# Optimization experiments

Hardware: AMD Instinct MI355X
Metric: run time of the kernel (lower is better)

The kernel has to match this reference:

```python
import jax, jax.numpy as jnp
import numpy as np

ITERATION = 10

def setup_inputs() -> dict:
    key = jax.random.key(0)
    k1, k2, k3 = jax.random.split(key, 3)
    a_inter = jax.random.normal(k1, (8, 64, 64, 32, 32), dtype=jnp.float32)
    logits = jax.random.normal(k2, (8, 64), dtype=jnp.float32)
    W = jax.random.normal(k3, (1, 64, 64), dtype=jnp.float32)
    return {"a_inter": a_inter, "logits": logits, "W": W}


def reference(a_inter, logits, W):
    N = W.shape[1]  # num_nodes
    B = a_inter.shape[0]
    # feats: [B, N, C*H*W]
    feats = a_inter[:, :, :N, :, :].reshape(B, N, -1)
    # expand logits [B, N] -> [B, N, N] (unsqueeze(1).expand in torch)
    logits0 = jnp.broadcast_to(logits[:, None, :], (B, N, N))

    feats_norm = jnp.linalg.norm(feats, ord=2, axis=2, keepdims=True)  # [B, N, 1]
    pairwise_norm = feats_norm @ jnp.swapaxes(feats_norm, 1, 2)        # [B, N, N]
    pairwise_dot = feats @ jnp.swapaxes(feats, 1, 2)                   # [B, N, N]
    pairwise_sim = pairwise_dot / (pairwise_norm + 1e-6)
    W_sym = (W + jnp.swapaxes(W, 1, 2)) / 2.0
    pairwise_potential = pairwise_sim * W_sym                          # [B, N, N]

    unary_potential = logits0

    def body(i, l):
        probs = jnp.swapaxes(jax.nn.sigmoid(l), 1, 2)  # [B, N, N]
        # probs*pp - (1-probs)*pp == (2*probs - 1)*pp
        pp_E = jnp.sum((2.0 * probs - 1.0) * pairwise_potential, axis=2, keepdims=True)
        return unary_potential + pp_E

    logits_out = jax.lax.fori_loop(0, ITERATION, body, logits0)
    return logits_out.mean(axis=1)  # [B, N]
```

## Files before the change

kernel.cpp:

```cpp
#include <hip/hip_runtime.h>
#include <math.h>

#define BATCH 8
#define NN 64
#define DD 65536
#define BPB 64
#define NBLK (BATCH * BPB)
#define KC (DD / BPB)
#define KW (KC / 4)
#define KSTEPS (KW / 32)
#define NTRI 10
#define PSZ (NTRI * 256)

typedef float  floatx4 __attribute__((ext_vector_type(4)));
typedef __bf16 bf16x8  __attribute__((ext_vector_type(8)));

static __device__ __forceinline__ bf16x8 cvt8(float4 lo, float4 hi) {
    const unsigned sel = 0x07060302u;
    union { unsigned u[4]; bf16x8 v; } r;
    r.u[0] = __builtin_amdgcn_perm(__float_as_uint(lo.y), __float_as_uint(lo.x), sel);
    r.u[1] = __builtin_amdgcn_perm(__float_as_uint(lo.w), __float_as_uint(lo.z), sel);
    r.u[2] = __builtin_amdgcn_perm(__float_as_uint(hi.y), __float_as_uint(hi.x), sel);
    r.u[3] = __builtin_amdgcn_perm(__float_as_uint(hi.w), __float_as_uint(hi.z), sel);
    return r.v;
}

__global__ __launch_bounds__(256, 3) void gram_partial_kernel(const float* __restrict__ a,
                                                              float* __restrict__ part) {
    __shared__ __align__(16) float red[3][NTRI][64][4];

    const int bid = blockIdx.x;
    const int b = bid >> 6;
    const int c = bid & (BPB - 1);

    const int tid  = threadIdx.x;
    const int w    = tid >> 6;
    const int lane = tid & 63;
    const int m    = lane & 15;
    const int q    = lane >> 4;

    const float* base = a + (size_t)b * NN * DD + (size_t)c * KC + (size_t)w * KW
                          + (size_t)m * DD + q * 8;
    const float* p0 = base;
    const float* p1 = base + (size_t)16 * DD;
    const float* p2 = base + (size_t)32 * DD;
    const float* p3 = base + (size_t)48 * DD;

    floatx4 acc[NTRI];
    #pragma unroll
    for (int i = 0; i < NTRI; ++i) acc[i] = (floatx4)0.0f;

    float4 A0, A1, A2, A3, A4, A5, A6, A7;
    float4 B0, B1, B2, B3, B4, B5, B6, B7;

#define LOADSET(R0,R1,R2,R3,R4,R5,R6,R7, o)                                \
    R0 = *(const float4*)(p0 + (o));  R1 = *(const float4*)(p0 + (o) + 4); \
    R2 = *(const float4*)(p1 + (o));  R3 = *(const float4*)(p1 + (o) + 4); \
    R4 = *(const float4*)(p2 + (o));  R5 = *(const float4*)(p2 + (o) + 4); \
    R6 = *(const float4*)(p3 + (o));  R7 = *(const float4*)(p3 + (o) + 4);

#define MFMASET(R0,R1,R2,R3,R4,R5,R6,R7)                                   \
    {                                                                      \
        bf16x8 f0 = cvt8(R0, R1);                                          \
        bf16x8 f1 = cvt8(R2, R3);                                          \
        bf16x8 f2 = cvt8(R4, R5);                                          \
        bf16x8 f3 = cvt8(R6, R7);                                          \
        acc[0] = __builtin_amdgcn_mfma_f32_16x16x32_bf16(f0, f0, acc[0], 0, 0, 0); \
        acc[1] = __builtin_amdgcn_mfma_f32_16x16x32_bf16(f0, f1, acc[1], 0, 0, 0); \
        acc[2] = __builtin_amdgcn_mfma_f32_16x16x32_bf16(f0, f2, acc[2], 0, 0, 0); \
        acc[3] = __builtin_amdgcn_mfma_f32_16x16x32_bf16(f0, f3, acc[3], 0, 0, 0); \
        acc[4] = __builtin_amdgcn_mfma_f32_16x16x32_bf16(f1, f1, acc[4], 0, 0, 0); \
        acc[5] = __builtin_amdgcn_mfma_f32_16x16x32_bf16(f1, f2, acc[5], 0, 0, 0); \
        acc[6] = __builtin_amdgcn_mfma_f32_16x16x32_bf16(f1, f3, acc[6], 0, 0, 0); \
        acc[7] = __builtin_amdgcn_mfma_f32_16x16x32_bf16(f2, f2, acc[7], 0, 0, 0); \
        acc[8] = __builtin_amdgcn_mfma_f32_16x16x32_bf16(f2, f3, acc[8], 0, 0, 0); \
        acc[9] = __builtin_amdgcn_mfma_f32_16x16x32_bf16(f3, f3, acc[9], 0, 0, 0); \
    }

    LOADSET(A0,A1,A2,A3,A4,A5,A6,A7, 0)
    #pragma unroll
    for (int s = 0; s < KSTEPS; s += 2) {
        LOADSET(B0,B1,B2,B3,B4,B5,B6,B7, (s + 1) * 32)
        MFMASET(A0,A1,A2,A3,A4,A5,A6,A7)
        if (s + 2 < KSTEPS) { LOADSET(A0,A1,A2,A3,A4,A5,A6,A7, (s + 2) * 32) }
        MFMASET(B0,B1,B2,B3,B4,B5,B6,B7)
    }
#undef LOADSET
#undef MFMASET

    if (w > 0) {
        #pragma unroll
        for (int t = 0; t < NTRI; ++t)
            *(floatx4*)&red[w - 1][t][lane][0] = acc[t];
    }
    __syncthreads();
    if (w == 0) {
        #pragma unroll
        for (int t = 0; t < NTRI; ++t) {
            floatx4 r0 = *(const floatx4*)&red[0][t][lane][0];
            floatx4 r1 = *(const floatx4*)&red[1][t][lane][0];
            floatx4 r2 = *(const floatx4*)&red[2][t][lane][0];
            acc[t] += (r0 + r1) + r2;
        }
        float* pg = part + (size_t)bid * PSZ;
        #pragma unroll
        for (int t = 0; t < NTRI; ++t) {
            float* tp = pg + t * 256 + m;
            #pragma unroll
            for (int r = 0; r < 4; ++r)
                tp[(q * 4 + r) * 16] = acc[t][r];
        }
    }
}

__global__ __launch_bounds__(128) void gram_reduce_kernel(const float* __restrict__ part,
                                                          float* __restrict__ gram) {
    const int gid = blockIdx.x * 128 + threadIdx.x;
    const int b   = gid >> 12;
    const int idx = gid & 4095;
    const int i   = idx >> 6;
    const int j   = idx & 63;
    const int ti  = i >> 4, tj = j >> 4;
    const int ib  = ti <= tj ? ti : tj;
    const int jb  = ti <= tj ? tj : ti;
    const int slot = ib * 4 - (ib * (ib - 1)) / 2 + (jb - ib);
    const int rr  = (ti <= tj) ? (i & 15) : (j & 15);
    const int cc  = (ti <= tj) ? (j & 15) : (i & 15);
    const int off = slot * 256 + rr * 16 + cc;
    const float* p = part + (size_t)b * BPB * PSZ + off;

    float s0 = 0.f, s1 = 0.f, s2 = 0.f, s3 = 0.f;
    #pragma unroll 4
    for (int c = 0; c < BPB; c += 4) {
        s0 += p[(size_t)(c + 0) * PSZ];
        s1 += p[(size_t)(c + 1) * PSZ];
        s2 += p[(size_t)(c + 2) * PSZ];
        s3 += p[(size_t)(c + 3) * PSZ];
    }
    gram[gid] = (s0 + s1) + (s2 + s3);
}

__global__ __launch_bounds__(256) void crf_kernel(const float* __restrict__ gram,
                                                  const float* __restrict__ logits,
                                                  const float* __restrict__ Wm,
                                                  float* __restrict__ out) {
    __shared__ float pp[NN][NN + 1];
    __shared__ float E[NN];
    __shared__ float nrm[NN];
    __shared__ float part[4 * NN];

    const int b  = blockIdx.x;
    const int tid = threadIdx.x;
    const int i  = tid & 63;
    const int jq = tid >> 6;
    const float* g = gram + b * NN * NN;

    if (jq == 0) nrm[i] = sqrtf(g[i * NN + i]);
    E[i] = 0.0f;
    __syncthreads();

    const float ni = nrm[i];
    for (int jj = 0; jj < 16; ++jj) {
        int j = jq * 16 + jj;
        float wsym = 0.5f * (Wm[i * NN + j] + Wm[j * NN + i]);
        pp[i][j] = g[i * NN + j] / (ni * nrm[j] + 1e-6f) * wsym;
    }
    const float li = logits[b * NN + i];
    __syncthreads();

    for (int it = 0; it < 10; ++it) {
        float acc = 0.0f;
        for (int jj = 0; jj < 16; ++jj) {
            int j = jq * 16 + jj;
            float t = li + E[j];
            float s = 1.0f / (1.0f + expf(-t));
            acc = fmaf(2.0f * s - 1.0f, pp[i][j], acc);
        }
        part[jq * NN + i] = acc;
        __syncthreads();
        if (jq == 0)
            E[i] = part[i] + part[NN + i] + part[2 * NN + i] + part[3 * NN + i];
        __syncthreads();
    }

    if (tid < 64) {
        float s = E[tid];
        for (int off = 32; off > 0; off >>= 1) s += __shfl_down(s, off);
        float meanE = __shfl(s, 0) * (1.0f / 64.0f);
        out[b * NN + tid] = logits[b * NN + tid] + meanE;
    }
}

extern "C" void kernel_launch(void* const* d_in, const int* in_sizes, int n_in,
                              void* d_out, int out_size, void* d_ws, size_t ws_size,
                              hipStream_t stream) {
    const float* a      = (const float*)d_in[0];
    const float* logits = (const float*)d_in[1];
    const float* Wm     = (const float*)d_in[2];
    float* out  = (float*)d_out;

    float* part = (float*)d_ws;
    float* gram = part + (size_t)NBLK * PSZ;

    gram_partial_kernel<<<NBLK, 256, 0, stream>>>(a, part);
    gram_reduce_kernel<<<(BATCH * NN * NN) / 128, 128, 0, stream>>>(part, gram);
    crf_kernel<<<BATCH, 256, 0, stream>>>(gram, logits, Wm, out);
}
```

Measured before the change: 217.7 us.

## Fuse gram reduction and CRF into partial kernel via atomics and last-block

Replaces the separate partial-store, reduce and CRF kernels with one fused kernel. Each block atomically adds its partial Gram tile into a per-batch accumulator, and the last block for each batch, found through an atomic counter, runs the CRF iterations. A small init kernel zeroes the accumulator and counters. This removes two launches and the partial-buffer round trip, at the cost of float atomics (non-deterministic summation order) and a serial CRF tail on a single block per batch.

After: 235.6 us. 1.08x slower.

```diff
diff --git a/kernel.cpp b/kernel.cpp
--- a/kernel.cpp
+++ b/kernel.cpp
@@ -11,6 +11,8 @@
 #define KSTEPS (KW / 32)
 #define NTRI 10
 #define PSZ (NTRI * 256)
+#define GRAM_FLOATS (BATCH * PSZ)
+#define INIT_N (GRAM_FLOATS + BATCH)
 
 typedef float  floatx4 __attribute__((ext_vector_type(4)));
 typedef __bf16 bf16x8  __attribute__((ext_vector_type(8)));
@@ -25,9 +27,26 @@
     return r.v;
 }
 
-__global__ __launch_bounds__(256, 3) void gram_partial_kernel(const float* __restrict__ a,
-                                                              float* __restrict__ part) {
-    __shared__ __align__(16) float red[3][NTRI][64][4];
+__global__ __launch_bounds__(256) void init_kernel(float* __restrict__ g) {
+    int i = blockIdx.x * 256 + threadIdx.x;
+    if (i < INIT_N) g[i] = 0.0f;
+}
+
+__global__ __launch_bounds__(256, 3) void fused_kernel(const float* __restrict__ a,
+                                                       const float* __restrict__ logits,
+                                                       const float* __restrict__ Wm,
+                                                       float* __restrict__ gram,
+                                                       float* __restrict__ out) {
+    __shared__ __align__(16) union {
+        float red[3][NTRI][64][4];
+        struct {
+            float G[NN][NN + 1];
+            float E[NN];
+            float nrm[NN];
+            float part[4 * NN];
+        } crf;
+    } sh;
+    __shared__ int lastFlag;
 
     const int bid = blockIdx.x;
     const int b = bid >> 6;
@@ -91,100 +110,86 @@
     if (w > 0) {
         #pragma unroll
         for (int t = 0; t < NTRI; ++t)
-            *(floatx4*)&red[w - 1][t][lane][0] = acc[t];
+            *(floatx4*)&sh.red[w - 1][t][lane][0] = acc[t];
     }
     __syncthreads();
     if (w == 0) {
         #pragma unroll
         for (int t = 0; t < NTRI; ++t) {
-            floatx4 r0 = *(const floatx4*)&red[0][t][lane][0];
-            floatx4 r1 = *(const floatx4*)&red[1][t][lane][0];
-            floatx4 r2 = *(const floatx4*)&red[2][t][lane][0];
+            floatx4 r0 = *(const floatx4*)&sh.red[0][t][lane][0];
+            floatx4 r1 = *(const floatx4*)&sh.red[1][t][lane][0];
+            floatx4 r2 = *(const floatx4*)&sh.red[2][t][lane][0];
             acc[t] += (r0 + r1) + r2;
         }
-        float* pg = part + (size_t)bid * PSZ;
+        float* pg = gram + (size_t)b * PSZ;
         #pragma unroll
         for (int t = 0; t < NTRI; ++t) {
             float* tp = pg + t * 256 + m;
             #pragma unroll
             for (int r = 0; r < 4; ++r)
-                tp[(q * 4 + r) * 16] = acc[t][r];
+                atomicAdd(&tp[(q * 4 + r) * 16], acc[t][r]);
         }
-    }
-}
-
-__global__ __launch_bounds__(128) void gram_reduce_kernel(const float* __restrict__ part,
-                                                          float* __restrict__ gram) {
-    const int gid = blockIdx.x * 128 + threadIdx.x;
-    const int b   = gid >> 12;
-    const int idx = gid & 4095;
-    const int i   = idx >> 6;
-    const int j   = idx & 63;
-    const int ti  = i >> 4, tj = j >> 4;
-    const int ib  = ti <= tj ? ti : tj;
-    const int jb  = ti <= tj ? tj : ti;
-    const int slot = ib * 4 - (ib * (ib - 1)) / 2 + (jb - ib);
-    const int rr  = (ti <= tj) ? (i & 15) : (j & 15);
-    const int cc  = (ti <= tj) ? (j & 15) : (i & 15);
-    const int off = slot * 256 + rr * 16 + cc;
-    const float* p = part + (size_t)b * BPB * PSZ + off;
-
-    float s0 = 0.f, s1 = 0.f, s2 = 0.f, s3 = 0.f;
-    #pragma unroll 4
-    for (int c = 0; c < BPB; c += 4) {
-        s0 += p[(size_t)(c + 0) * PSZ];
-        s1 += p[(size_t)(c + 1) * PSZ];
-        s2 += p[(size_t)(c + 2) * PSZ];
-        s3 += p[(size_t)(c + 3) * PSZ];
-    }
-    gram[gid] = (s0 + s1) + (s2 + s3);
-}
-
-__global__ __launch_bounds__(256) void crf_kernel(const float* __restrict__ gram,
-                                                  const float* __restrict__ logits,
-                                                  const float* __restrict__ Wm,
-                                                  float* __restrict__ out) {
-    __shared__ float pp[NN][NN + 1];
-    __shared__ float E[NN];
-    __shared__ float nrm[NN];
-    __shared__ float part[4 * NN];
-
-    const int b  = blockIdx.x;
-    const int tid = threadIdx.x;
-    const int i  = tid & 63;
+        __threadfence();
+    }
+    if (tid == 0) {
+        unsigned* cnt = (unsigned*)(gram + GRAM_FLOATS);
+        unsigned old = atomicAdd(cnt + b, 1u);
+        lastFlag = (old == BPB - 1) ? 1 : 0;
+    }
+    __syncthreads();
+    if (!lastFlag) return;
+
+    const float* gb = gram + (size_t)b * PSZ;
+    for (int idx = tid; idx < NN * NN; idx += 256) {
+        int i  = idx >> 6, j = idx & 63;
+        int ti = i >> 4, tj = j >> 4;
+        int ib = ti <= tj ? ti : tj;
+        int jb = ti <= tj ? tj : ti;
+        int slot = ib * 4 - (ib * (ib - 1)) / 2 + (jb - ib);
+        int rr = (ti <= tj) ? (i & 15) : (j & 15);
+        int cc = (ti <= tj) ? (j & 15) : (i & 15);
+        float v = __hip_atomic_load(gb + slot * 256 + rr * 16 + cc,
+                                    __ATOMIC_RELAXED, __HIP_MEMORY_SCOPE_AGENT);
+        sh.crf.G[i][j] = v;
+    }
+    __syncthreads();
+
+    const int ci = tid & 63;
     const int jq = tid >> 6;
-    const float* g = gram + b * NN * NN;
-
-    if (jq == 0) nrm[i] = sqrtf(g[i * NN + i]);
-    E[i] = 0.0f;
-    __syncthreads();
-
-    const float ni = nrm[i];
+
+    if (jq == 0) sh.crf.nrm[ci] = sqrtf(sh.crf.G[ci][ci]);
+    sh.crf.E[ci] = 0.0f;
+    __syncthreads();
+
+    const float ni = sh.crf.nrm[ci];
+    #pragma unroll
     for (int jj = 0; jj < 16; ++jj) {
         int j = jq * 16 + jj;
-        float wsym = 0.5f * (Wm[i * NN + j] + Wm[j * NN + i]);
-        pp[i][j] = g[i * NN + j] / (ni * nrm[j] + 1e-6f) * wsym;
-    }
-    const float li = logits[b * NN + i];
+        float wsym = 0.5f * (Wm[ci * NN + j] + Wm[j * NN + ci]);
+        sh.crf.G[ci][j] = sh.crf.G[ci][j] / (ni * sh.crf.nrm[j] + 1e-6f) * wsym;
+    }
+    const float li = logits[b * NN + ci];
     __syncthreads();
 
     for (int it = 0; it < 10; ++it) {
-        float acc = 0.0f;
+        float acc2 = 0.0f;
+        #pragma unroll
         for (int jj = 0; jj < 16; ++jj) {
             int j = jq * 16 + jj;
-            float t = li + E[j];
+            float t = li + sh.crf.E[j];
             float s = 1.0f / (1.0f + expf(-t));
-            acc = fmaf(2.0f * s - 1.0f, pp[i][j], acc);
+            acc2 = fmaf(2.0f * s - 1.0f, sh.crf.G[ci][j], acc2);
         }
-        part[jq * NN + i] = acc;
+        sh.crf.part[jq * NN + ci] = acc2;
         __syncthreads();
         if (jq == 0)
-            E[i] = part[i] + part[NN + i] + part[2 * NN + i] + part[3 * NN + i];
+            sh.crf.E[ci] = sh.crf.part[ci] + sh.crf.part[NN + ci]
+                         + sh.crf.part[2 * NN + ci] + sh.crf.part[3 * NN + ci];
         __syncthreads();
     }
 
     if (tid < 64) {
-        float s = E[tid];
+        float s = sh.crf.E[tid];
         for (int off = 32; off > 0; off >>= 1) s += __shfl_down(s, off);
         float meanE = __shfl(s, 0) * (1.0f / 64.0f);
         out[b * NN + tid] = logits[b * NN + tid] + meanE;
@@ -199,10 +204,8 @@
     const float* Wm     = (const float*)d_in[2];
     float* out  = (float*)d_out;
 
-    float* part = (float*)d_ws;
-    float* gram = part + (size_t)NBLK * PSZ;
-
-    gram_partial_kernel<<<NBLK, 256, 0, stream>>>(a, part);
-    gram_reduce_kernel<<<(BATCH * NN * NN) / 128, 128, 0, stream>>>(part, gram);
-    crf_kernel<<<BATCH, 256, 0, stream>>>(gram, logits, Wm, out);
-}
+    float* gram = (float*)d_ws;
+
+    init_kernel<<<(INIT_N + 255) / 256, 256, 0, stream>>>(gram);
+    fused_kernel<<<NBLK, 256, 0, stream>>>(a, logits, Wm, gram, out);
+}
```

## Split Gram partials per wave and drop the in-block LDS reduction

Applied to the files above, without the earlier changes.

The Gram partial kernel now launches 2048 blocks of 128 threads instead of 512 blocks of 256. Each wave covers a 128-element K slice and writes its own partial tile straight to global memory, so the shared-memory reduction and its barrier are gone. The reduce kernel now sums 512 partials per batch instead of 64, using eight accumulators. The aim is more waves in flight to hide load latency, but the partial buffer grows eightfold, adding a lot of global write and read traffic plus a longer strided reduction.

New measurement: 261.1 us. 19.9% more time.

```diff
diff --git a/kernel.cpp b/kernel.cpp
--- a/kernel.cpp
+++ b/kernel.cpp
@@ -4,11 +4,11 @@
 #define BATCH 8
 #define NN 64
 #define DD 65536
-#define BPB 64
-#define NBLK (BATCH * BPB)
-#define KC (DD / BPB)
-#define KW (KC / 4)
-#define KSTEPS (KW / 32)
+#define NBLK 2048
+#define WPB 512
+#define NWAVE (BATCH * WPB)
+#define KWV 128
+#define KSTEPS (KWV / 32)
 #define NTRI 10
 #define PSZ (NTRI * 256)
 
@@ -25,21 +25,18 @@
     return r.v;
 }
 
-__global__ __launch_bounds__(256, 3) void gram_partial_kernel(const float* __restrict__ a,
+__global__ __launch_bounds__(128, 4) void gram_partial_kernel(const float* __restrict__ a,
                                                               float* __restrict__ part) {
-    __shared__ __align__(16) float red[3][NTRI][64][4];
-
-    const int bid = blockIdx.x;
-    const int b = bid >> 6;
-    const int c = bid & (BPB - 1);
-
+    const int bid  = blockIdx.x;
+    const int b    = bid >> 8;
     const int tid  = threadIdx.x;
     const int w    = tid >> 6;
     const int lane = tid & 63;
     const int m    = lane & 15;
     const int q    = lane >> 4;
+    const int c    = ((bid & 255) << 1) | w;
 
-    const float* base = a + (size_t)b * NN * DD + (size_t)c * KC + (size_t)w * KW
+    const float* base = a + (size_t)b * NN * DD + (size_t)c * KWV
                           + (size_t)m * DD + q * 8;
     const float* p0 = base;
     const float* p1 = base + (size_t)16 * DD;
@@ -88,28 +85,13 @@
 #undef LOADSET
 #undef MFMASET
 
-    if (w > 0) {
+    float* pg = part + ((size_t)b * WPB + c) * PSZ;
+    #pragma unroll
+    for (int t = 0; t < NTRI; ++t) {
+        float* tp = pg + t * 256 + m;
         #pragma unroll
-        for (int t = 0; t < NTRI; ++t)
-            *(floatx4*)&red[w - 1][t][lane][0] = acc[t];
-    }
-    __syncthreads();
-    if (w == 0) {
-        #pragma unroll
-        for (int t = 0; t < NTRI; ++t) {
-            floatx4 r0 = *(const floatx4*)&red[0][t][lane][0];
-            floatx4 r1 = *(const floatx4*)&red[1][t][lane][0];
-            floatx4 r2 = *(const floatx4*)&red[2][t][lane][0];
-            acc[t] += (r0 + r1) + r2;
-        }
-        float* pg = part + (size_t)bid * PSZ;
-        #pragma unroll
-        for (int t = 0; t < NTRI; ++t) {
-            float* tp = pg + t * 256 + m;
-            #pragma unroll
-            for (int r = 0; r < 4; ++r)
-                tp[(q * 4 + r) * 16] = acc[t][r];
-        }
+        for (int r = 0; r < 4; ++r)
+            tp[(q * 4 + r) * 16] = acc[t][r];
     }
 }
 
@@ -127,17 +109,22 @@
     const int rr  = (ti <= tj) ? (i & 15) : (j & 15);
     const int cc  = (ti <= tj) ? (j & 15) : (i & 15);
     const int off = slot * 256 + rr * 16 + cc;
-    const float* p = part + (size_t)b * BPB * PSZ + off;
+    const float* p = part + (size_t)b * WPB * PSZ + off;
 
     float s0 = 0.f, s1 = 0.f, s2 = 0.f, s3 = 0.f;
+    float s4 = 0.f, s5 = 0.f, s6 = 0.f, s7 = 0.f;
     #pragma unroll 4
-    for (int c = 0; c < BPB; c += 4) {
+    for (int c = 0; c < WPB; c += 8) {
         s0 += p[(size_t)(c + 0) * PSZ];
         s1 += p[(size_t)(c + 1) * PSZ];
         s2 += p[(size_t)(c + 2) * PSZ];
         s3 += p[(size_t)(c + 3) * PSZ];
+        s4 += p[(size_t)(c + 4) * PSZ];
+        s5 += p[(size_t)(c + 5) * PSZ];
+        s6 += p[(size_t)(c + 6) * PSZ];
+        s7 += p[(size_t)(c + 7) * PSZ];
     }
-    gram[gid] = (s0 + s1) + (s2 + s3);
+    gram[gid] = ((s0 + s1) + (s2 + s3)) + ((s4 + s5) + (s6 + s7));
 }
 
 __global__ __launch_bounds__(256) void crf_kernel(const float* __restrict__ gram,
@@ -200,9 +187,9 @@
     float* out  = (float*)d_out;
 
     float* part = (float*)d_ws;
-    float* gram = part + (size_t)NBLK * PSZ;
+    float* gram = part + (size_t)NWAVE * PSZ;
 
-    gram_partial_kernel<<<NBLK, 256, 0, stream>>>(a, part);
+    gram_partial_kernel<<<NBLK, 128, 0, stream>>>(a, part);
     gram_reduce_kernel<<<(BATCH * NN * NN) / 128, 128, 0, stream>>>(part, gram);
     crf_kernel<<<BATCH, 256, 0, stream>>>(gram, logits, Wm, out);
 }
```
